# Kernel optimization log

Measured on AMD Instinct MI355X. Metric: run time of the kernel, lower is better.

The kernel has to match this reference:

```python
import jax, jax.numpy as jnp
import numpy as np

H, Dh = 8, 16          # heads, per-head dim (out_channels=128)
F_OUT = H * Dh
NEG_SLOPE = 0.2        # PyG GAT-style leaky_relu slope


def setup_inputs() -> dict:
    key = jax.random.key(0)
    ks = jax.random.split(key, 20)
    Ns, Nc, Ecs, Ess, Din, C = 100000, 100000, 500000, 500000, 64, 2
    s = 0.1
    return {
        "x_subject": jax.random.normal(ks[0], (Ns, Din), jnp.float32),
        "x_channel": jax.random.normal(ks[1], (Nc, Din), jnp.float32),
        "edge_cs": jax.random.randint(ks[2], (2, Ecs), 0, Ns, jnp.int32),
        "edge_ss": jax.random.randint(ks[3], (2, Ess), 0, Ns, jnp.int32),
        "W_subj": s * jax.random.normal(ks[4], (Din, F_OUT), jnp.float32),
        "b_subj": jnp.zeros((F_OUT,), jnp.float32),
        "W_chan": s * jax.random.normal(ks[5], (Din, F_OUT), jnp.float32),
        "b_chan": jnp.zeros((F_OUT,), jnp.float32),
        "att_src_cs": s * jax.random.normal(ks[6], (H, Dh), jnp.float32),
        "att_dst_cs": s * jax.random.normal(ks[7], (H, Dh), jnp.float32),
        "att_src_ss": s * jax.random.normal(ks[8], (H, Dh), jnp.float32),
        "att_dst_ss": s * jax.random.normal(ks[9], (H, Dh), jnp.float32),
        "k_w": s * jax.random.normal(ks[10], (F_OUT, F_OUT), jnp.float32),
        "k_b": jnp.zeros((F_OUT,), jnp.float32),
        "q": s * jax.random.normal(ks[11], (F_OUT,), jnp.float32),
        "lin_w": s * jax.random.normal(ks[12], (F_OUT, C), jnp.float32),
        "lin_b": jnp.zeros((C,), jnp.float32),
    }


def _edge_softmax(alpha, dst, num_seg):
    # alpha: [E, H]; numerically stable softmax over edges grouped by dst node
    m = jax.ops.segment_max(alpha, dst, num_segments=num_seg)
    e = jnp.exp(alpha - m[dst])
    s = jax.ops.segment_sum(e, dst, num_segments=num_seg)
    return e / (s[dst] + 1e-16)


def _han_edge_type(x_src, x_dst, att_src, att_dst, edge, n_dst):
    # GAT-style attention of one edge type (PyG HANConv.propagate)
    a_src = jnp.einsum('nhd,hd->nh', x_src, att_src)   # [N_src, H]
    a_dst = jnp.einsum('nhd,hd->nh', x_dst, att_dst)   # [N_dst, H]
    src, dst = edge[0], edge[1]
    alpha = jax.nn.leaky_relu(a_src[src] + a_dst[dst], NEG_SLOPE)  # [E, H]
    alpha = _edge_softmax(alpha, dst, n_dst)
    msg = x_src[src] * alpha[:, :, None]               # [E, H, Dh]
    out = jax.ops.segment_sum(msg, dst, num_segments=n_dst)
    return jax.nn.relu(out.reshape(n_dst, F_OUT))


def reference(x_subject, x_channel, edge_cs, edge_ss,
              W_subj, b_subj, W_chan, b_chan,
              att_src_cs, att_dst_cs, att_src_ss, att_dst_ss,
              k_w, k_b, q, lin_w, lin_b):
    Ns = x_subject.shape[0]
    Nc = x_channel.shape[0]
    hs = (x_subject @ W_subj + b_subj).reshape(Ns, H, Dh)
    hc = (x_channel @ W_chan + b_chan).reshape(Nc, H, Dh)

    # per-metapath outputs for dst type SUBJECT (dropout omitted: eval mode)
    o1 = _han_edge_type(hc, hs, att_src_cs, att_dst_cs, edge_cs, Ns)
    o2 = _han_edge_type(hs, hs, att_src_ss, att_dst_ss, edge_ss, Ns)

    # semantic attention across metapaths (PyG HANConv.group)
    outs = jnp.stack([o1, o2])                             # [M, Ns, F]
    score = jnp.einsum('f,mf->m', q, jnp.tanh(outs @ k_w + k_b).mean(axis=1))
    attn = jax.nn.softmax(score)                           # [M]
    fused = jnp.einsum('m,mnf->nf', attn, outs)            # [Ns, F]

    return fused @ lin_w + lin_b                           # [Ns, dim_out]
```

## Files before the change

### kernel.cpp

```cpp
#include <hip/hip_runtime.h>

#define HH 8
#define FOUT 128
#define DIN 64
#define NCOL 160
#define NSLOPE 0.2f
#define HR 8192
#define CHUNKN 20

typedef __attribute__((ext_vector_type(8))) short bf16x8;
typedef __attribute__((ext_vector_type(4))) float f32x4;

__device__ __forceinline__ float fast_rcp(float x) { return __builtin_amdgcn_rcpf(x); }

__device__ __forceinline__ float fast_tanh(float x) {
    float ax = fabsf(x);
    float e = __expf(-2.f * ax);
    float r = (1.f - e) * fast_rcp(1.f + e);
    return x >= 0.f ? r : -r;
}

__device__ __forceinline__ unsigned short f2bf(float f) {
    unsigned u = __builtin_bit_cast(unsigned, f);
    unsigned r = (u + 0x7fffu + ((u >> 16) & 1u)) >> 16;
    return (unsigned short)r;
}

__device__ __forceinline__ float bf2f(unsigned short u) {
    return __builtin_bit_cast(float, (unsigned)u << 16);
}

__global__ __launch_bounds__(256) void k_linm(
    const float* __restrict__ x0, const float* __restrict__ W0, const float* __restrict__ b0,
    const float* __restrict__ A00, const float* __restrict__ A01, const float* __restrict__ A02,
    unsigned short* __restrict__ h0,
    float* __restrict__ a00, float* __restrict__ a01, float* __restrict__ a02, int N0, int natt0,
    const float* __restrict__ x1, const float* __restrict__ W1, const float* __restrict__ b1,
    const float* __restrict__ A10, const float* __restrict__ A11, const float* __restrict__ A12,
    unsigned short* __restrict__ h1,
    float* __restrict__ a10, float* __restrict__ a11, float* __restrict__ a12, int N1, int natt1)
{
    const int y = blockIdx.y;
    const float* __restrict__ x  = y ? x1 : x0;
    const float* __restrict__ W  = y ? W1 : W0;
    const float* __restrict__ b  = y ? b1 : b0;
    const float* __restrict__ at0 = y ? A10 : A00;
    const float* __restrict__ at1 = y ? A11 : A01;
    const float* __restrict__ at2 = y ? A12 : A02;
    unsigned short* __restrict__ hb = y ? h1 : h0;
    float* __restrict__ a0 = y ? a10 : a00;
    float* __restrict__ a1 = y ? a11 : a01;
    float* __restrict__ a2 = y ? a12 : a02;
    const int N = y ? N1 : N0;
    const int natt = y ? natt1 : natt0;

    __shared__ unsigned short wtl[NCOL * DIN];
    __shared__ float attl[3][FOUT];
    __shared__ float bl[FOUT];
    __shared__ float abias[32];
    const int tid = threadIdx.x;

    if (tid < FOUT) {
        bl[tid] = b[tid];
        attl[0][tid] = at0[tid];
        attl[1][tid] = at1[tid];
        attl[2][tid] = at2[tid];
    }
    __syncthreads();

    for (int idx = tid; idx < DIN * FOUT; idx += 256) {
        int fi = idx >> 7, fo = idx & 127;
        wtl[fo * DIN + (((fi >> 3) ^ (fo & 7)) << 3) + (fi & 7)] = f2bf(W[idx]);
    }
    for (int idx = tid; idx < 2048; idx += 256) {
        int fi = idx >> 5, cs = idx & 31;
        float acc = 0.f;
        if (cs < 24) {
            int a = cs >> 3, hd = cs & 7;
            #pragma unroll
            for (int d = 0; d < 16; d++)
                acc += W[fi * FOUT + hd * 16 + d] * attl[a][hd * 16 + d];
        }
        int fo = 128 + cs;
        wtl[fo * DIN + (((fi >> 3) ^ (fo & 7)) << 3) + (fi & 7)] =
            cs < 24 ? f2bf(acc) : (unsigned short)0;
    }
    if (tid < 32) {
        float acc = 0.f;
        if (tid < 24) {
            int a = tid >> 3, hd = tid & 7;
            #pragma unroll
            for (int d = 0; d < 16; d++) acc += b[hd * 16 + d] * attl[a][hd * 16 + d];
        }
        abias[tid] = acc;
    }
    __syncthreads();

    const int w = tid >> 6, lane = tid & 63;
    const int rt = blockIdx.x * 4 + w;
    if (rt * 16 >= N) return;
    const int r16 = lane & 15, g = lane >> 4;

    int node = rt * 16 + r16;
    if (node >= N) node = N - 1;
    const float* xr = x + (size_t)node * DIN;
    bf16x8 af[2];
    #pragma unroll
    for (int kk = 0; kk < 2; kk++) {
        float4 v0 = *(const float4*)(xr + kk * 32 + g * 8);
        float4 v1 = *(const float4*)(xr + kk * 32 + g * 8 + 4);
        bf16x8 f;
        f[0] = (short)f2bf(v0.x); f[1] = (short)f2bf(v0.y);
        f[2] = (short)f2bf(v0.z); f[3] = (short)f2bf(v0.w);
        f[4] = (short)f2bf(v1.x); f[5] = (short)f2bf(v1.y);
        f[6] = (short)f2bf(v1.z); f[7] = (short)f2bf(v1.w);
        af[kk] = f;
    }

    #pragma unroll
    for (int j = 0; j < 10; j++) {
        const int fo = j * 16 + r16;
        f32x4 acc = {0.f, 0.f, 0.f, 0.f};
        #pragma unroll
        for (int kk = 0; kk < 2; kk++) {
            int c = (kk * 4 + g) ^ (fo & 7);
            bf16x8 bfr = *(bf16x8*)&wtl[fo * DIN + c * 8];
            acc = __builtin_amdgcn_mfma_f32_16x16x32_bf16(af[kk], bfr, acc, 0, 0, 0);
        }
        if (j < 8) {
            float bv = bl[fo];
            #pragma unroll
            for (int r = 0; r < 4; r++) {
                int nr = rt * 16 + g * 4 + r;
                if (nr < N) hb[(size_t)nr * FOUT + fo] = f2bf(acc[r] + bv);
            }
        } else {
            int cs = (j - 8) * 16 + r16;
            if (cs < 24) {
                int a = cs >> 3;
                if (a < natt) {
                    float* __restrict__ ga = a == 0 ? a0 : (a == 1 ? a1 : a2);
                    int hd = cs & 7;
                    float ab = abias[cs];
                    #pragma unroll
                    for (int r = 0; r < 4; r++) {
                        int nr = rt * 16 + g * 4 + r;
                        if (nr < N) ga[(size_t)nr * HH + hd] = acc[r] + ab;
                    }
                }
            }
        }
    }
}

__global__ __launch_bounds__(512) void k_hist(
    const int* __restrict__ e0, int E0, const int* __restrict__ e1, int E1,
    int* __restrict__ chist, int nbin, int nbp)
{
    const int bx = blockIdx.x;
    const int chunk = bx / nbp;
    const int tb = bx % nbp;
    if (tb >= 2 * nbin) return;
    const bool type = tb >= nbin;
    const int bin = type ? tb - nbin : tb;
    const int* __restrict__ e = type ? e1 : e0;
    const int E = type ? E1 : E0;
    const int lo = bin * HR;

    __shared__ int hist[HR];
    for (int j = threadIdx.x; j < HR; j += 512) hist[j] = 0;
    __syncthreads();

    const int per = (E + CHUNKN - 1) / CHUNKN;
    const int s0 = chunk * per;
    const int s1 = s0 + per < E ? s0 + per : E;
    for (int i = s0 + threadIdx.x; i < s1; i += 512) {
        unsigned r = (unsigned)(e[E + i] - lo);
        if (r < HR) atomicAdd(&hist[r], 1);
    }
    __syncthreads();
    int* __restrict__ out = chist + ((size_t)tb * CHUNKN + chunk) * HR;
    for (int j = threadIdx.x; j < HR; j += 512) out[j] = hist[j];
}

__global__ __launch_bounds__(256) void k_scan_block2(
    int* __restrict__ chist,
    int* __restrict__ out0, int* __restrict__ bs0,
    int* __restrict__ out1, int* __restrict__ bs1,
    int* __restrict__ d0, int* __restrict__ d1,
    int n, int nbin)
{
    const int type = blockIdx.y;
    int* __restrict__ out = type ? out1 : out0;
    int* __restrict__ bsum = type ? bs1 : bs0;
    int* __restrict__ deg = type ? d1 : d0;
    __shared__ int s[256];
    const int tid = threadIdx.x;
    const int i = blockIdx.x * 256 + tid;
    int v = 0;
    int hvals[CHUNKN];
    int* hp = nullptr;
    if (i < n) {
        const int bin = i / HR, jr = i & (HR - 1);
        hp = chist + ((size_t)(type * nbin + bin) * CHUNKN) * HR + jr;
        #pragma unroll
        for (int c = 0; c < CHUNKN; c++) { hvals[c] = hp[c * HR]; v += hvals[c]; }
    }
    s[tid] = v; __syncthreads();
    for (int off = 1; off < 256; off <<= 1) {
        int t = tid >= off ? s[tid - off] : 0;
        __syncthreads();
        s[tid] += t;
        __syncthreads();
    }
    if (i < n) {
        out[i] = s[tid] - v;
        deg[i] = v;
        int run = 0;
        #pragma unroll
        for (int c = 0; c < CHUNKN; c++) { int t = hvals[c]; hp[c * HR] = run; run += t; }
    }
    if (tid == 255) bsum[blockIdx.x] = s[255];
}

__global__ __launch_bounds__(256) void k_scan_add2(
    int* __restrict__ o0, const int* __restrict__ b0,
    int* __restrict__ o1, const int* __restrict__ b1, int n)
{
    int* __restrict__ out = blockIdx.y ? o1 : o0;
    const int* __restrict__ bsum = blockIdx.y ? b1 : b0;
    __shared__ int s[256];
    const int tid = threadIdx.x;
    const int bx = blockIdx.x;
    int acc = 0;
    for (int j = tid; j < bx; j += 256) acc += bsum[j];
    s[tid] = acc; __syncthreads();
    for (int w = 128; w > 0; w >>= 1) {
        if (tid < w) s[tid] += s[tid + w];
        __syncthreads();
    }
    const int pre = s[0];
    const int i = bx * 256 + tid;
    if (i < n) out[i] += pre;
}

__global__ __launch_bounds__(512) void k_scatb(
    const int* __restrict__ e0, int E0, const int* __restrict__ rp0, int* __restrict__ sl0,
    const int* __restrict__ e1, int E1, const int* __restrict__ rp1, int* __restrict__ sl1,
    const int* __restrict__ chist, int nbin, int nbp)
{
    const int bx = blockIdx.x;
    const int chunk = bx / nbp;
    const int tb = bx % nbp;
    if (tb >= 2 * nbin) return;
    const bool type = tb >= nbin;
    const int bin = type ? tb - nbin : tb;
    const int* __restrict__ e = type ? e1 : e0;
    const int E = type ? E1 : E0;
    const int* __restrict__ rp = type ? rp1 : rp0;
    int* __restrict__ sl = type ? sl1 : sl0;
    const int lo = bin * HR;

    __shared__ int cnt[HR];
    const int* __restrict__ cop = chist + ((size_t)tb * CHUNKN + chunk) * HR;
    for (int j = threadIdx.x; j < HR; j += 512) cnt[j] = cop[j];
    __syncthreads();

    const int per = (E + CHUNKN - 1) / CHUNKN;
    const int s0 = chunk * per;
    const int s1 = s0 + per < E ? s0 + per : E;
    for (int i = s0 + threadIdx.x; i < s1; i += 512) {
        int dst = e[E + i];
        unsigned r = (unsigned)(dst - lo);
        if (r < HR) {
            int pos = rp[dst] + atomicAdd(&cnt[r], 1);
            sl[pos] = e[i];
        }
    }
}

__global__ __launch_bounds__(256) void k_agg2(
    const int* __restrict__ sl0, const int* __restrict__ rp0, const int* __restrict__ dg0,
    const unsigned short* __restrict__ xb0, const float* __restrict__ as0, const float* __restrict__ ad0,
    unsigned short* __restrict__ oo0,
    const int* __restrict__ sl1, const int* __restrict__ rp1, const int* __restrict__ dg1,
    const unsigned short* __restrict__ xb1, const float* __restrict__ as1, const float* __restrict__ ad1,
    unsigned short* __restrict__ oo1,
    int N)
{
    const bool m = blockIdx.y;
    const int* __restrict__ sl = m ? sl1 : sl0;
    const int* __restrict__ rp = m ? rp1 : rp0;
    const int* __restrict__ dg = m ? dg1 : dg0;
    const unsigned short* __restrict__ xb = m ? xb1 : xb0;
    const float* __restrict__ as_ = m ? as1 : as0;
    const float* __restrict__ ad_ = m ? ad1 : ad0;
    unsigned short* __restrict__ oo = m ? oo1 : oo0;

    const int t = blockIdx.x * 256 + threadIdx.x;
    const int dst = t >> 5;
    if (dst >= N) return;
    const int lane = t & 31;
    const int h = lane >> 2;
    const int d = dg[dst];
    const int base = rp[dst];
    const float adv = ad_[(size_t)dst * HH + h];
    float acc0 = 0.f, acc1 = 0.f, acc2 = 0.f, acc3 = 0.f;
    float wsum = 0.f;
    int src_next = d > 0 ? sl[base] : 0;
    for (int k = 0; k < d; k++) {
        int src = src_next;
        if (k + 1 < d) src_next = sl[base + k + 1];
        float a = as_[(size_t)src * HH + h] + adv;
        a = a > 0.f ? a : NSLOPE * a;
        float wv = __expf(a);
        uint2 xv = *(const uint2*)(xb + (size_t)src * FOUT + lane * 4);
        acc0 = fmaf(wv, bf2f((unsigned short)(xv.x & 0xffff)), acc0);
        acc1 = fmaf(wv, bf2f((unsigned short)(xv.x >> 16)), acc1);
        acc2 = fmaf(wv, bf2f((unsigned short)(xv.y & 0xffff)), acc2);
        acc3 = fmaf(wv, bf2f((unsigned short)(xv.y >> 16)), acc3);
        wsum += wv;
    }
    float inv = fast_rcp(wsum + 1e-16f);
    unsigned p0 = ((unsigned)f2bf(fmaxf(acc1 * inv, 0.f)) << 16) | f2bf(fmaxf(acc0 * inv, 0.f));
    unsigned p1 = ((unsigned)f2bf(fmaxf(acc3 * inv, 0.f)) << 16) | f2bf(fmaxf(acc2 * inv, 0.f));
    *(uint2*)(oo + (size_t)dst * FOUT + lane * 4) = make_uint2(p0, p1);
}

__global__ __launch_bounds__(256) void k_sem(
    const unsigned short* __restrict__ o1p, const unsigned short* __restrict__ o2p,
    const float* __restrict__ kw, const float* __restrict__ kb,
    const float* __restrict__ q, float* __restrict__ score, int N)
{
    __shared__ unsigned short kwl[FOUT * FOUT];
    __shared__ float red[256];
    const int tid = threadIdx.x;

    for (int idx = tid; idx < FOUT * FOUT; idx += 256) {
        int fi = idx >> 7, fo = idx & 127;
        int c = (fi >> 3) ^ (fo & 15);
        kwl[fo * 128 + c * 8 + (fi & 7)] = f2bf(kw[idx]);
    }
    __syncthreads();

    const int lane = tid & 63;
    const int w = tid >> 6;
    const int n0 = blockIdx.x * 256 + w * 64;
    const int r16 = lane & 15;
    const int g = lane >> 4;

    float qv[8], kbv[8];
    #pragma unroll
    for (int j = 0; j < 8; j++) { qv[j] = q[j * 16 + r16]; kbv[j] = kb[j * 16 + r16]; }

    for (int m = 0; m < 2; m++) {
        const unsigned short* __restrict__ o = m ? o2p : o1p;
        bf16x8 afrag[4][4];
        #pragma unroll
        for (int i = 0; i < 4; i++) {
            int node = n0 + i * 16 + r16;
            if (node > N - 1) node = N - 1;
            const unsigned short* rowp = o + (size_t)node * FOUT + g * 8;
            #pragma unroll
            for (int kk = 0; kk < 4; kk++)
                afrag[i][kk] = *(const bf16x8*)(rowp + kk * 32);
        }

        float part = 0.f;
        #pragma unroll
        for (int j = 0; j < 8; j++) {
            const int fo = j * 16 + r16;
            f32x4 acc0 = {0.f,0.f,0.f,0.f}, acc1 = {0.f,0.f,0.f,0.f};
            f32x4 acc2 = {0.f,0.f,0.f,0.f}, acc3 = {0.f,0.f,0.f,0.f};
            #pragma unroll
            for (int kk = 0; kk < 4; kk++) {
                int c = (kk * 4 + g) ^ (fo & 15);
                bf16x8 bfr = *(bf16x8*)&kwl[fo * 128 + c * 8];
                acc0 = __builtin_amdgcn_mfma_f32_16x16x32_bf16(afrag[0][kk], bfr, acc0, 0, 0, 0);
                acc1 = __builtin_amdgcn_mfma_f32_16x16x32_bf16(afrag[1][kk], bfr, acc1, 0, 0, 0);
                acc2 = __builtin_amdgcn_mfma_f32_16x16x32_bf16(afrag[2][kk], bfr, acc2, 0, 0, 0);
                acc3 = __builtin_amdgcn_mfma_f32_16x16x32_bf16(afrag[3][kk], bfr, acc3, 0, 0, 0);
            }
            #pragma unroll
            for (int i = 0; i < 4; i++) {
                f32x4 a = i == 0 ? acc0 : (i == 1 ? acc1 : (i == 2 ? acc2 : acc3));
                #pragma unroll
                for (int r = 0; r < 4; r++) {
                    int node = n0 + i * 16 + g * 4 + r;
                    if (node < N) part += fast_tanh(a[r] + kbv[j]) * qv[j];
                }
            }
        }
        red[tid] = part;
        __syncthreads();
        for (int s2 = 128; s2 > 0; s2 >>= 1) {
            if (tid < s2) red[tid] += red[tid + s2];
            __syncthreads();
        }
        if (tid == 0) atomicAdd(score + m, red[0]);
        __syncthreads();
    }
}

__global__ __launch_bounds__(256) void k_final(
    const unsigned short* __restrict__ o1, const unsigned short* __restrict__ o2,
    const float* __restrict__ score, float invN,
    const float* __restrict__ lw, const float* __restrict__ lb,
    float* __restrict__ out, int N)
{
    __shared__ float lwl[FOUT * 2];
    __shared__ float attns[2];
    const int tid = threadIdx.x;
    if (tid < FOUT * 2) lwl[tid] = lw[tid];
    if (tid == 0) {
        float s0 = score[0] * invN, s1 = score[1] * invN;
        float mm = fmaxf(s0, s1);
        float e0 = __expf(s0 - mm), e1 = __expf(s1 - mm);
        float inv = 1.f / (e0 + e1);
        attns[0] = e0 * inv;
        attns[1] = e1 * inv;
    }
    __syncthreads();
    const int n = blockIdx.x * 256 + tid;
    if (n >= N) return;
    const float a0 = attns[0], a1 = attns[1];
    float acc0 = lb[0], acc1 = lb[1];
    const uint4* p1 = (const uint4*)(o1 + (size_t)n * FOUT);
    const uint4* p2 = (const uint4*)(o2 + (size_t)n * FOUT);
    #pragma unroll
    for (int i = 0; i < FOUT / 8; i++) {
        uint4 v1 = p1[i];
        uint4 v2 = p2[i];
        const unsigned w1[4] = {v1.x, v1.y, v1.z, v1.w};
        const unsigned w2[4] = {v2.x, v2.y, v2.z, v2.w};
        #pragma unroll
        for (int c = 0; c < 4; c++) {
            int f = i * 8 + c * 2;
            float f0 = a0 * bf2f((unsigned short)(w1[c] & 0xffff)) +
                       a1 * bf2f((unsigned short)(w2[c] & 0xffff));
            float f1 = a0 * bf2f((unsigned short)(w1[c] >> 16)) +
                       a1 * bf2f((unsigned short)(w2[c] >> 16));
            acc0 += f0 * lwl[f*2]   + f1 * lwl[(f+1)*2];
            acc1 += f0 * lwl[f*2+1] + f1 * lwl[(f+1)*2+1];
        }
    }
    *(float2*)(out + (size_t)n * 2) = make_float2(acc0, acc1);
}

extern "C" void kernel_launch(void* const* d_in, const int* in_sizes, int n_in,
                              void* d_out, int out_size, void* d_ws, size_t ws_size,
                              hipStream_t stream)
{
    const float* x_subj = (const float*)d_in[0];
    const float* x_chan = (const float*)d_in[1];
    const int*   e_cs   = (const int*)d_in[2];
    const int*   e_ss   = (const int*)d_in[3];
    const float* W_s    = (const float*)d_in[4];
    const float* b_s    = (const float*)d_in[5];
    const float* W_c    = (const float*)d_in[6];
    const float* b_c    = (const float*)d_in[7];
    const float* att_src_cs = (const float*)d_in[8];
    const float* att_dst_cs = (const float*)d_in[9];
    const float* att_src_ss = (const float*)d_in[10];
    const float* att_dst_ss = (const float*)d_in[11];
    const float* k_w  = (const float*)d_in[12];
    const float* k_b  = (const float*)d_in[13];
    const float* q    = (const float*)d_in[14];
    const float* lw   = (const float*)d_in[15];
    const float* lb   = (const float*)d_in[16];

    const int Ns  = in_sizes[0] / DIN;
    const int Nc  = in_sizes[1] / DIN;
    const int Ecs = in_sizes[2] / 2;
    const int Ess = in_sizes[3] / 2;

    const int nbin = (Ns + HR - 1) / HR;
    const int nbp = ((2 * nbin + 7) / 8) * 8;

    char* p = (char*)d_ws;
    unsigned short* hbf_s = (unsigned short*)p; p += (size_t)Ns * FOUT * 2;
    unsigned short* hbf_c = (unsigned short*)p; p += (size_t)Nc * FOUT * 2;
    float* a_src_cs_ = (float*)p; p += (size_t)Nc * HH * 4;
    float* a_dst_cs_ = (float*)p; p += (size_t)Ns * HH * 4;
    float* a_src_ss_ = (float*)p; p += (size_t)Ns * HH * 4;
    float* a_dst_ss_ = (float*)p; p += (size_t)Ns * HH * 4;
    unsigned short* o1 = (unsigned short*)p; p += (size_t)Ns * FOUT * 2;
    unsigned short* o2 = (unsigned short*)p; p += (size_t)Ns * FOUT * 2;
    int* srclist_cs  = (int*)p;   p += (size_t)Ecs * 4;
    int* srclist_ss  = (int*)p;   p += (size_t)Ess * 4;
    int* rowptr_cs   = (int*)p;   p += (size_t)Ns * 4;
    int* rowptr_ss   = (int*)p;   p += (size_t)Ns * 4;
    int* deg_cs      = (int*)p;   p += (size_t)Ns * 4;
    int* deg_ss      = (int*)p;   p += (size_t)Ns * 4;
    int* bsum0       = (int*)p;   p += 2048;
    int* bsum1       = (int*)p;   p += 2048;
    int* chist       = (int*)p;   p += (size_t)2 * nbin * CHUNKN * HR * 4;
    float* score = (float*)p; p += 16;
    hipMemsetAsync(score, 0, 16, stream);

    const int nbN = (Ns + 255) / 256;
    const int Nmax = Ns > Nc ? Ns : Nc;
    const int gx_lin = ((Nmax + 15) / 16 + 3) / 4;

    k_linm<<<dim3(gx_lin, 2), dim3(256), 0, stream>>>(
        x_subj, W_s, b_s, att_dst_cs, att_src_ss, att_dst_ss,
        hbf_s, a_dst_cs_, a_src_ss_, a_dst_ss_, Ns, 3,
        x_chan, W_c, b_c, att_src_cs, att_src_cs, att_src_cs,
        hbf_c, a_src_cs_, a_src_cs_, a_src_cs_, Nc, 1);

    k_hist<<<dim3(nbp * CHUNKN), dim3(512), 0, stream>>>(
        e_cs, Ecs, e_ss, Ess, chist, nbin, nbp);
    k_scan_block2<<<dim3(nbN, 2), dim3(256), 0, stream>>>(
        chist, rowptr_cs, bsum0, rowptr_ss, bsum1, deg_cs, deg_ss, Ns, nbin);
    k_scan_add2<<<dim3(nbN, 2), dim3(256), 0, stream>>>(rowptr_cs, bsum0, rowptr_ss, bsum1, Ns);
    k_scatb<<<dim3(nbp * CHUNKN), dim3(512), 0, stream>>>(
        e_cs, Ecs, rowptr_cs, srclist_cs,
        e_ss, Ess, rowptr_ss, srclist_ss, chist, nbin, nbp);

    k_agg2<<<dim3(((size_t)Ns * 32 + 255) / 256, 2), dim3(256), 0, stream>>>(
        srclist_cs, rowptr_cs, deg_cs, hbf_c, a_src_cs_, a_dst_cs_, o1,
        srclist_ss, rowptr_ss, deg_ss, hbf_s, a_src_ss_, a_dst_ss_, o2, Ns);

    k_sem<<<dim3(nbN), dim3(256), 0, stream>>>(o1, o2, k_w, k_b, q, score, Ns);
    k_final<<<dim3(nbN), dim3(256), 0, stream>>>(
        o1, o2, score, 1.f / (float)Ns, lw, lb, (float*)d_out, Ns);
}
```

Measured before the change: 233.2 us.

## Fold final linear projection into semantic-attention MFMA pass via extra output columns

Uses linearity (fused@lin_w = a0*(o1@lin_w)+a1*(o2@lin_w)) to compute the per-metapath projections o1@lin_w and o2@lin_w inside k_sem as a ninth 16-column MFMA tile appended to k_w in LDS. k_final then only reads two small float2 vectors per node instead of re-reading both bf16 o1/o2 rows. This removes a full pass over o1/o2 from k_final at the cost of one extra MFMA tile, a larger LDS buffer, and small scattered z writes in k_sem. The projection weights are now applied in bf16 rather than fp32.

```diff
diff --git a/kernel.cpp b/kernel.cpp
--- a/kernel.cpp
+++ b/kernel.cpp
@@ -4,6 +4,7 @@
 #define FOUT 128
 #define DIN 64
 #define NCOL 160
+#define SEMR 144
 #define NSLOPE 0.2f
 #define HR 8192
 #define CHUNKN 20
@@ -330,9 +331,10 @@
 __global__ __launch_bounds__(256) void k_sem(
     const unsigned short* __restrict__ o1p, const unsigned short* __restrict__ o2p,
     const float* __restrict__ kw, const float* __restrict__ kb,
-    const float* __restrict__ q, float* __restrict__ score, int N)
-{
-    __shared__ unsigned short kwl[FOUT * FOUT];
+    const float* __restrict__ q, const float* __restrict__ lw,
+    float* __restrict__ score, float* __restrict__ z1p, float* __restrict__ z2p, int N)
+{
+    __shared__ unsigned short kwl[SEMR * FOUT];
     __shared__ float red[256];
     const int tid = threadIdx.x;
 
@@ -340,6 +342,13 @@
         int fi = idx >> 7, fo = idx & 127;
         int c = (fi >> 3) ^ (fo & 15);
         kwl[fo * 128 + c * 8 + (fi & 7)] = f2bf(kw[idx]);
+    }
+    for (int idx = tid; idx < (SEMR - FOUT) * FOUT; idx += 256) {
+        int fi = idx & 127, fr = idx >> 7;
+        int fo = FOUT + fr;
+        int c = (fi >> 3) ^ (fo & 15);
+        float v = fr == 0 ? lw[fi * 2] : (fr == 1 ? lw[fi * 2 + 1] : 0.f);
+        kwl[fo * 128 + c * 8 + (fi & 7)] = f2bf(v);
     }
     __syncthreads();
 
@@ -355,6 +364,7 @@
 
     for (int m = 0; m < 2; m++) {
         const unsigned short* __restrict__ o = m ? o2p : o1p;
+        float* __restrict__ zp = m ? z2p : z1p;
         bf16x8 afrag[4][4];
         #pragma unroll
         for (int i = 0; i < 4; i++) {
@@ -368,7 +378,7 @@
 
         float part = 0.f;
         #pragma unroll
-        for (int j = 0; j < 8; j++) {
+        for (int j = 0; j < 9; j++) {
             const int fo = j * 16 + r16;
             f32x4 acc0 = {0.f,0.f,0.f,0.f}, acc1 = {0.f,0.f,0.f,0.f};
             f32x4 acc2 = {0.f,0.f,0.f,0.f}, acc3 = {0.f,0.f,0.f,0.f};
@@ -384,10 +394,18 @@
             #pragma unroll
             for (int i = 0; i < 4; i++) {
                 f32x4 a = i == 0 ? acc0 : (i == 1 ? acc1 : (i == 2 ? acc2 : acc3));
-                #pragma unroll
-                for (int r = 0; r < 4; r++) {
-                    int node = n0 + i * 16 + g * 4 + r;
-                    if (node < N) part += fast_tanh(a[r] + kbv[j]) * qv[j];
+                if (j < 8) {
+                    #pragma unroll
+                    for (int r = 0; r < 4; r++) {
+                        int node = n0 + i * 16 + g * 4 + r;
+                        if (node < N) part += fast_tanh(a[r] + kbv[j]) * qv[j];
+                    }
+                } else if (r16 < 2) {
+                    #pragma unroll
+                    for (int r = 0; r < 4; r++) {
+                        int node = n0 + i * 16 + g * 4 + r;
+                        if (node < N) zp[(size_t)node * 2 + r16] = a[r];
+                    }
                 }
             }
         }
@@ -403,15 +421,12 @@
 }
 
 __global__ __launch_bounds__(256) void k_final(
-    const unsigned short* __restrict__ o1, const unsigned short* __restrict__ o2,
+    const float* __restrict__ z1, const float* __restrict__ z2,
     const float* __restrict__ score, float invN,
-    const float* __restrict__ lw, const float* __restrict__ lb,
-    float* __restrict__ out, int N)
-{
-    __shared__ float lwl[FOUT * 2];
+    const float* __restrict__ lb, float* __restrict__ out, int N)
+{
     __shared__ float attns[2];
     const int tid = threadIdx.x;
-    if (tid < FOUT * 2) lwl[tid] = lw[tid];
     if (tid == 0) {
         float s0 = score[0] * invN, s1 = score[1] * invN;
         float mm = fmaxf(s0, s1);
@@ -424,27 +439,12 @@
     const int n = blockIdx.x * 256 + tid;
     if (n >= N) return;
     const float a0 = attns[0], a1 = attns[1];
-    float acc0 = lb[0], acc1 = lb[1];
-    const uint4* p1 = (const uint4*)(o1 + (size_t)n * FOUT);
-    const uint4* p2 = (const uint4*)(o2 + (size_t)n * FOUT);
-    #pragma unroll
-    for (int i = 0; i < FOUT / 8; i++) {
-        uint4 v1 = p1[i];
-        uint4 v2 = p2[i];
-        const unsigned w1[4] = {v1.x, v1.y, v1.z, v1.w};
-        const unsigned w2[4] = {v2.x, v2.y, v2.z, v2.w};
-        #pragma unroll
-        for (int c = 0; c < 4; c++) {
-            int f = i * 8 + c * 2;
-            float f0 = a0 * bf2f((unsigned short)(w1[c] & 0xffff)) +
-                       a1 * bf2f((unsigned short)(w2[c] & 0xffff));
-            float f1 = a0 * bf2f((unsigned short)(w1[c] >> 16)) +
-                       a1 * bf2f((unsigned short)(w2[c] >> 16));
-            acc0 += f0 * lwl[f*2]   + f1 * lwl[(f+1)*2];
-            acc1 += f0 * lwl[f*2+1] + f1 * lwl[(f+1)*2+1];
-        }
-    }
-    *(float2*)(out + (size_t)n * 2) = make_float2(acc0, acc1);
+    float2 v1 = *(const float2*)(z1 + (size_t)n * 2);
+    float2 v2 = *(const float2*)(z2 + (size_t)n * 2);
+    float2 o;
+    o.x = a0 * v1.x + a1 * v2.x + lb[0];
+    o.y = a0 * v1.y + a1 * v2.y + lb[1];
+    *(float2*)(out + (size_t)n * 2) = o;
 }
 
 extern "C" void kernel_launch(void* const* d_in, const int* in_sizes, int n_in,
@@ -492,6 +492,8 @@
     int* rowptr_ss   = (int*)p;   p += (size_t)Ns * 4;
     int* deg_cs      = (int*)p;   p += (size_t)Ns * 4;
     int* deg_ss      = (int*)p;   p += (size_t)Ns * 4;
+    float* z1        = (float*)p; p += (size_t)Ns * 2 * 4;
+    float* z2        = (float*)p; p += (size_t)Ns * 2 * 4;
     int* bsum0       = (int*)p;   p += 2048;
     int* bsum1       = (int*)p;   p += 2048;
     int* chist       = (int*)p;   p += (size_t)2 * nbin * CHUNKN * HR * 4;
@@ -521,7 +523,8 @@
         srclist_cs, rowptr_cs, deg_cs, hbf_c, a_src_cs_, a_dst_cs_, o1,
         srclist_ss, rowptr_ss, deg_ss, hbf_s, a_src_ss_, a_dst_ss_, o2, Ns);
 
-    k_sem<<<dim3(nbN), dim3(256), 0, stream>>>(o1, o2, k_w, k_b, q, score, Ns);
+    k_sem<<<dim3(nbN), dim3(256), 0, stream>>>(
+        o1, o2, k_w, k_b, q, lw, score, z1, z2, Ns);
     k_final<<<dim3(nbN), dim3(256), 0, stream>>>(
-        o1, o2, score, 1.f / (float)Ns, lw, lb, (float*)d_out, Ns);
-}
+        z1, z2, score, 1.f / (float)Ns, lb, (float*)d_out, Ns);
+}
```

Result: faster. 220.2 us (-5.6%).
